# Kernel tuning notes

Hardware: AMD Instinct MI355X
Metric: run time of the kernel (lower is better)

The kernel has to match this reference:

```python
import jax, jax.numpy as jnp
import numpy as np
import math

B, S, D, H = 2, 2048, 1024, 16
HD = D // H  # 64 head features


def setup_inputs() -> dict:
    key = jax.random.key(0)
    ks = jax.random.split(key, 6)
    x = jax.random.normal(ks[0], (B, S, D), jnp.float32)
    wq = jax.random.normal(ks[1], (D, D), jnp.float32) * 0.02
    wk = jax.random.normal(ks[2], (D, D), jnp.float32) * 0.02
    wv = jax.random.normal(ks[3], (D, D), jnp.float32) * 0.02
    wo = jax.random.normal(ks[4], (D, D), jnp.float32) * 0.02
    # Llama-style RoPE frequencies: unit-modulus complex per (pos, pair),
    # stored as separate cos/sin arrays of shape [S, HD//2].
    inv_freq = 1.0 / (10000.0 ** (jnp.arange(0, HD, 2, dtype=jnp.float32) / HD))
    ang = jnp.arange(S, dtype=jnp.float32)[:, None] * inv_freq[None, :]
    freq_cos = jnp.cos(ang)
    freq_sin = jnp.sin(ang)
    # realistic padding: each sequence keeps a random prefix of at least S//2 tokens
    lengths = jax.random.randint(ks[5], (B,), S // 2, S + 1)
    padding_mask = (jnp.arange(S)[None, :] < lengths[:, None]).astype(jnp.int32)
    return dict(x=x, wq=wq, wk=wk, wv=wv, wo=wo,
                freq_cos=freq_cos, freq_sin=freq_sin, padding_mask=padding_mask)


def _apply_rope(t, cos, sin):
    # t: [B, S, H, HD]; cos/sin: [S, HD//2]
    tr = t.reshape(t.shape[:-1] + (HD // 2, 2))
    t0, t1 = tr[..., 0], tr[..., 1]
    c = cos[None, :, None, :]
    s = sin[None, :, None, :]
    o0 = t0 * c - t1 * s  # real part of complex multiply
    o1 = t0 * s + t1 * c  # imag part
    return jnp.stack([o0, o1], axis=-1).reshape(t.shape)


def reference(x, wq, wk, wv, wo, freq_cos, freq_sin, padding_mask):
    # QKV projections (torch Linear: y = x @ W.T, no bias)
    q = (x @ wq.T).reshape(B, S, H, HD)
    k = (x @ wk.T).reshape(B, S, H, HD)
    v = (x @ wv.T).reshape(B, S, H, HD)
    q = _apply_rope(q, freq_cos, freq_sin)
    k = _apply_rope(k, freq_cos, freq_sin)
    q = jnp.transpose(q, (0, 2, 1, 3))  # [B,H,S,HD]
    k = jnp.transpose(k, (0, 2, 1, 3))
    v = jnp.transpose(v, (0, 2, 1, 3))
    # NOTE: original scales by sqrt(n_features), not sqrt(head_dim)
    scores = jnp.einsum('bhqd,bhkd->bhqk', q, k) / math.sqrt(D)
    bias = jnp.where(padding_mask[:, None, None, :] == 0,
                     jnp.float32(-jnp.inf), jnp.float32(0.0))
    p = jax.nn.softmax(scores + bias, axis=-1)
    out = jnp.einsum('bhqk,bhkd->bhqd', p, v)
    out = jnp.transpose(out, (0, 2, 1, 3)).reshape(B, S, D)
    return out @ wo.T
```

## Files before the change

kernel.cpp:

```cpp
#include <hip/hip_runtime.h>
#include <hip/hip_bf16.h>
#include <stdint.h>

typedef unsigned short u16;
typedef __attribute__((ext_vector_type(8))) short bf16x8;
typedef __attribute__((ext_vector_type(4))) float f32x4;
typedef __attribute__((ext_vector_type(16))) float f32x16;

__device__ __forceinline__ u16 f2bf(float f) {
  union { float f; uint32_t u; } a; a.f = f;
  return (u16)((a.u + 0x7FFFu + ((a.u >> 16) & 1u)) >> 16);
}

__device__ __forceinline__ void gload_lds16(const void* g, void* l) {
  auto* gp = (__attribute__((address_space(1))) void*)(uintptr_t)g;
  auto* lp = (__attribute__((address_space(3))) void*)(uintptr_t)l;
  __builtin_amdgcn_global_load_lds(gp, lp, 16, 0, 0);
}

__device__ __forceinline__ float exp2_fast(float x) {
  float r;
  asm("v_exp_f32 %0, %1" : "=v"(r) : "v"(x));
  return r;
}

template <int N> __device__ __forceinline__ void waitvm() {
  if constexpr (N == 3)      asm volatile("s_waitcnt vmcnt(3)" ::: "memory");
  else if constexpr (N == 4) asm volatile("s_waitcnt vmcnt(4)" ::: "memory");
  else                       asm volatile("s_waitcnt vmcnt(0)" ::: "memory");
}

#define CVTPK(d, a, b) asm("v_cvt_pk_bf16_f32 %0, %1, %2" : "=v"(d) : "v"(a), "v"(b))
#define SWAP32(a, b)   asm("v_permlane32_swap_b32 %0, %1" : "+v"(a), "+v"(b))
#define BARRIER() do { asm volatile("" ::: "memory"); __builtin_amdgcn_s_barrier(); asm volatile("" ::: "memory"); } while (0)

__global__ void cvt_kernel(const float4* __restrict__ x, const float4* __restrict__ wq,
                           const float4* __restrict__ wk, const float4* __restrict__ wv,
                           const float4* __restrict__ wo,
                           ushort4* __restrict__ xb, ushort4* __restrict__ wqkv,
                           ushort4* __restrict__ wob) {
  const int XN = (2 * 2048 * 1024) / 4;
  const int WN = (1024 * 1024) / 4;
  const int total = XN + 4 * WN;
  for (int i = blockIdx.x * 256 + threadIdx.x; i < total; i += gridDim.x * 256) {
    float4 v; ushort4* dst;
    if (i < XN) { v = x[i]; dst = xb + i; }
    else {
      int j = i - XN; int m = j >> 18; int o = j & (WN - 1);
      const float4* src = (m == 0) ? wq : (m == 1) ? wk : (m == 2) ? wv : wo;
      v = src[o];
      dst = (m < 3) ? (wqkv + j) : (wob + o);
    }
    ushort4 r; r.x = f2bf(v.x); r.y = f2bf(v.y); r.z = f2bf(v.z); r.w = f2bf(v.w);
    *dst = r;
  }
}

__global__ void len_kernel(const int* __restrict__ mask, int* __restrict__ lens) {
  __shared__ int red[256];
  int b = blockIdx.x, s = 0;
  for (int i = threadIdx.x; i < 2048; i += 256) s += mask[b * 2048 + i];
  red[threadIdx.x] = s;
  __syncthreads();
  if (threadIdx.x < 64) {
    int v = red[threadIdx.x] + red[threadIdx.x + 64] + red[threadIdx.x + 128] + red[threadIdx.x + 192];
    #pragma unroll
    for (int o = 32; o > 0; o >>= 1) v += __shfl_down(v, o);
    if (threadIdx.x == 0) lens[b] = v;
  }
}

template <int BM, int BN, int MODE>
__global__ __launch_bounds__(256, 3)
void gemm3(const u16* __restrict__ A, const u16* __restrict__ Bm,
           int nTm, float* __restrict__ outf,
           u16* __restrict__ Qb, u16* __restrict__ Kb, u16* __restrict__ VbT,
           const float* __restrict__ cosT, const float* __restrict__ sinT) {
  constexpr int MREP = BM / 32;
  constexpr int NREP = BN / 32;
  constexpr int LA = BM / 64;
  constexpr int LB = BN / 64;
  constexpr int LOADS = LA + LB;
  __shared__ alignas(16) u16 SA[3][BM * 32];
  __shared__ alignas(16) u16 SB[3][BN * 32];

  const int tid = threadIdx.x, lane = tid & 63, wid = tid >> 6;
  const int wm = (wid >> 1) * (BM / 2), wn = (wid & 1) * (BN / 2);
  const int lr = lane & 15, lg = lane >> 4;

  const int cpx = gridDim.x >> 3;
  const int bid = (blockIdx.x & 7) * cpx + (blockIdx.x >> 3);
  const int m0 = (bid % nTm) * BM;
  const int n0 = (bid / nTm) * BN;

  const int srow = tid >> 2;
  const int schunk = (tid & 3) ^ ((srow >> 1) & 3);
  const u16* gA = A + (int64_t)(m0 + srow) * 1024 + schunk * 8;
  const u16* gB = Bm + (int64_t)(n0 + srow) * 1024 + schunk * 8;
  const int sdst = wid * 512;

#define STAGE(b, t) do { const int _ko = (t) * 32; \
    _Pragma("unroll") for (int j = 0; j < LA; ++j) \
      gload_lds16(gA + (int64_t)(j * 64) * 1024 + _ko, &SA[b][j * 2048 + sdst]); \
    _Pragma("unroll") for (int j = 0; j < LB; ++j) \
      gload_lds16(gB + (int64_t)(j * 64) * 1024 + _ko, &SB[b][j * 2048 + sdst]); } while (0)

  f32x4 acc[MREP][NREP];
  #pragma unroll
  for (int i = 0; i < MREP; ++i)
    #pragma unroll
    for (int j = 0; j < NREP; ++j)
      #pragma unroll
      for (int e = 0; e < 4; ++e) acc[i][j][e] = 0.0f;

  const int rchunk = (lg ^ ((lr >> 1) & 3)) * 8;

  STAGE(0, 0);
  STAGE(1, 1);
  waitvm<LOADS>();
  BARRIER();

  int bc = 0, bs = 2;
  for (int t = 0; t < 32; ++t) {
    if (t < 30) STAGE(bs, t + 2);
    const u16* sa = SA[bc];
    const u16* sb = SB[bc];
    bf16x8 af[MREP], bfm[NREP];
    #pragma unroll
    for (int i = 0; i < MREP; ++i) af[i] = *(const bf16x8*)&sa[(wm + i * 16 + lr) * 32 + rchunk];
    #pragma unroll
    for (int i = 0; i < NREP; ++i) bfm[i] = *(const bf16x8*)&sb[(wn + i * 16 + lr) * 32 + rchunk];
    #pragma unroll
    for (int mi = 0; mi < MREP; ++mi)
      #pragma unroll
      for (int ni = 0; ni < NREP; ++ni)
        acc[mi][ni] = __builtin_amdgcn_mfma_f32_16x16x32_bf16(af[mi], bfm[ni], acc[mi][ni], 0, 0, 0);
    if (t < 30) waitvm<LOADS>();
    else        waitvm<0>();
    BARRIER();
    bc = (bc == 2) ? 0 : bc + 1;
    bs = (bs == 2) ? 0 : bs + 1;
  }

  if (MODE == 0) {
    #pragma unroll
    for (int mi = 0; mi < MREP; ++mi)
      #pragma unroll
      for (int r = 0; r < 4; ++r) {
        const int row = m0 + wm + mi * 16 + lg * 4 + r;
        float* orow = outf + (int64_t)row * 1024 + n0 + wn + lr;
        #pragma unroll
        for (int ni = 0; ni < NREP; ++ni) orow[ni * 16] = acc[mi][ni][r];
      }
  } else {
    #pragma unroll
    for (int mi = 0; mi < MREP; ++mi) {
      #pragma unroll
      for (int r = 0; r < 4; ++r) {
        const int row = m0 + wm + mi * 16 + lg * 4 + r;
        const int bb = row >> 11, ss = row & 2047;
        #pragma unroll
        for (int ni = 0; ni < NREP; ++ni) {
          const int n = n0 + wn + ni * 16 + lr;
          float v = acc[mi][ni][r];
          if (n < 2048) {
            float partner = __shfl_xor(v, 1);
            const int ii = (n >> 1) & 31;
            const float c = cosT[ss * 32 + ii];
            const float sn = sinT[ss * 32 + ii];
            float rv = (n & 1) ? (partner * sn + v * c) : (v * c - partner * sn);
            const int h = (n >> 6) & 15, d = n & 63;
            const int idx = ((bb * 16 + h) * 2048 + ss) * 64 + d;
            if (n < 1024) Qb[idx] = f2bf(rv * 0.0450842298f);
            else          Kb[idx] = f2bf(rv);
          } else {
            const int n2 = n - 2048;
            const int h = n2 >> 6, d = n2 & 63;
            VbT[((int64_t)(bb * 16 + h) * 64 + d) * 2048 + ss] = f2bf(v);
          }
        }
      }
    }
  }
#undef STAGE
}

__global__ __launch_bounds__(256, 2)
void attn_kernel(const u16* __restrict__ Qb, const u16* __restrict__ Kb,
                 const u16* __restrict__ VbT, u16* __restrict__ attnb,
                 const int* __restrict__ lens) {
  __shared__ alignas(16) u16 Klds[2][64 * 64];
  __shared__ alignas(16) u16 Vlds[2][64 * 64];
  const int tid = threadIdx.x, lane = tid & 63, wid = tid >> 6;
  const int hi = lane >> 5, ql = lane & 31;
  const int bh = blockIdx.x >> 4;
  const int len = lens[bh >> 4];
  const int qrow = (blockIdx.x & 15) * 128 + wid * 32 + ql;

  bf16x8 qf[4];
  const u16* qptr = Qb + ((int64_t)bh * 2048 + qrow) * 64 + hi * 8;
  #pragma unroll
  for (int c = 0; c < 4; ++c) qf[c] = *(const bf16x8*)(qptr + c * 16);

  const int srow = tid >> 3, schunk = (tid & 7) ^ (srow & 7);
  const u16* kg = Kb + ((int64_t)bh * 2048 + srow) * 64 + schunk * 8;
  const u16* vg = VbT + ((int64_t)bh * 64 + srow) * 2048 + schunk * 8;
  const int dstoff = wid * 512;

  f32x16 oacc[2];
  #pragma unroll
  for (int r = 0; r < 16; ++r) { oacc[0][r] = 0.0f; oacc[1][r] = 0.0f; }
  float mrun = -1e30f, lrun = 0.0f;

  const int nt = (len + 63) >> 6;
  gload_lds16(kg,             &Klds[0][dstoff]);
  gload_lds16(kg + 32 * 64,   &Klds[0][2048 + dstoff]);
  gload_lds16(vg,             &Vlds[0][dstoff]);
  gload_lds16(vg + 32 * 2048, &Vlds[0][2048 + dstoff]);
  __syncthreads();

  const u16* kgn = kg + 64 * 64;
  const u16* vgn = vg + 64;

  for (int t = 0; t < nt; ++t) {
    const int bu = t & 1;
    if (t + 1 < nt) {
      gload_lds16(kgn,             &Klds[bu ^ 1][dstoff]);
      gload_lds16(kgn + 32 * 64,   &Klds[bu ^ 1][2048 + dstoff]);
      gload_lds16(vgn,             &Vlds[bu ^ 1][dstoff]);
      gload_lds16(vgn + 32 * 2048, &Vlds[bu ^ 1][2048 + dstoff]);
    }
    kgn += 64 * 64; vgn += 64;

    f32x16 s0, s1;
    #pragma unroll
    for (int r = 0; r < 16; ++r) { s0[r] = 0.0f; s1[r] = 0.0f; }
    __builtin_amdgcn_s_setprio(1);
    #pragma unroll
    for (int c = 0; c < 4; ++c) {
      const int slot = (((2 * c + hi) ^ (ql & 7)) * 8);
      bf16x8 kf0 = *(const bf16x8*)&Klds[bu][ql * 64 + slot];
      bf16x8 kf1 = *(const bf16x8*)&Klds[bu][(32 + ql) * 64 + slot];
      s0 = __builtin_amdgcn_mfma_f32_32x32x16_bf16(kf0, qf[c], s0, 0, 0, 0);
      s1 = __builtin_amdgcn_mfma_f32_32x32x16_bf16(kf1, qf[c], s1, 0, 0, 0);
    }
    __builtin_amdgcn_s_setprio(0);

    const int k0 = t * 64;
    if (k0 + 64 > len) {
      #pragma unroll
      for (int r = 0; r < 16; ++r) {
        const int key = k0 + (r & 3) + 8 * (r >> 2) + 4 * hi;
        if (key >= len) s0[r] = -1e30f;
        if (key + 32 >= len) s1[r] = -1e30f;
      }
    }

    float ma = fmaxf(s0[0], s1[0]), mb = fmaxf(s0[1], s1[1]);
    float mc = fmaxf(s0[2], s1[2]), md = fmaxf(s0[3], s1[3]);
    #pragma unroll
    for (int r = 4; r < 16; r += 4) {
      ma = fmaxf(ma, fmaxf(s0[r], s1[r]));
      mb = fmaxf(mb, fmaxf(s0[r + 1], s1[r + 1]));
      mc = fmaxf(mc, fmaxf(s0[r + 2], s1[r + 2]));
      md = fmaxf(md, fmaxf(s0[r + 3], s1[r + 3]));
    }
    float mx = fmaxf(fmaxf(ma, mb), fmaxf(mc, md));
    mx = fmaxf(mx, __shfl_xor(mx, 32));
    if (!__all(mx - mrun <= 11.0f)) {
      const float mnew = fmaxf(mrun, mx);
      const float sc = exp2_fast(mrun - mnew);
      #pragma unroll
      for (int r = 0; r < 16; ++r) { oacc[0][r] *= sc; oacc[1][r] *= sc; }
      lrun *= sc;
      mrun = mnew;
    }
    float p[32];
    float ps0 = 0.0f, ps1 = 0.0f, ps2 = 0.0f, ps3 = 0.0f;
    #pragma unroll
    for (int r = 0; r < 16; r += 4) {
      p[r]      = exp2_fast(s0[r] - mrun);
      p[r + 1]  = exp2_fast(s0[r + 1] - mrun);
      p[r + 2]  = exp2_fast(s0[r + 2] - mrun);
      p[r + 3]  = exp2_fast(s0[r + 3] - mrun);
      p[16 + r]     = exp2_fast(s1[r] - mrun);
      p[16 + r + 1] = exp2_fast(s1[r + 1] - mrun);
      p[16 + r + 2] = exp2_fast(s1[r + 2] - mrun);
      p[16 + r + 3] = exp2_fast(s1[r + 3] - mrun);
      ps0 += p[r] + p[16 + r];
      ps1 += p[r + 1] + p[16 + r + 1];
      ps2 += p[r + 2] + p[16 + r + 2];
      ps3 += p[r + 3] + p[16 + r + 3];
    }
    float psum = (ps0 + ps1) + (ps2 + ps3);
    psum += __shfl_xor(psum, 32);
    lrun += psum;

    bf16x8 pfrag[4];
    #pragma unroll
    for (int ks = 0; ks < 4; ++ks) {
      uint32_t a0, a1, a2, a3;
      CVTPK(a0, p[8 * ks + 0], p[8 * ks + 1]);
      CVTPK(a1, p[8 * ks + 2], p[8 * ks + 3]);
      CVTPK(a2, p[8 * ks + 4], p[8 * ks + 5]);
      CVTPK(a3, p[8 * ks + 6], p[8 * ks + 7]);
      SWAP32(a0, a2);
      SWAP32(a1, a3);
      union { uint32_t u[4]; bf16x8 v; } pw;
      pw.u[0] = a0; pw.u[1] = a1; pw.u[2] = a2; pw.u[3] = a3;
      pfrag[ks] = pw.v;
    }

    __builtin_amdgcn_s_setprio(1);
    #pragma unroll
    for (int dc = 0; dc < 2; ++dc) {
      const int drow = dc * 32 + ql;
      #pragma unroll
      for (int ks = 0; ks < 4; ++ks) {
        const int slot = (((2 * ks + hi) ^ (ql & 7)) * 8);
        bf16x8 vf = *(const bf16x8*)&Vlds[bu][drow * 64 + slot];
        oacc[dc] = __builtin_amdgcn_mfma_f32_32x32x16_bf16(vf, pfrag[ks], oacc[dc], 0, 0, 0);
      }
    }
    __builtin_amdgcn_s_setprio(0);
    __syncthreads();
  }

  const float inv = 1.0f / lrun;
  u16* outp = attnb + ((int64_t)((bh >> 4) * 2048 + qrow)) * 1024 + (bh & 15) * 64;
  #pragma unroll
  for (int dc = 0; dc < 2; ++dc)
    #pragma unroll
    for (int g = 0; g < 4; ++g) {
      ushort4 w;
      w.x = f2bf(oacc[dc][4 * g + 0] * inv);
      w.y = f2bf(oacc[dc][4 * g + 1] * inv);
      w.z = f2bf(oacc[dc][4 * g + 2] * inv);
      w.w = f2bf(oacc[dc][4 * g + 3] * inv);
      *(ushort4*)(outp + dc * 32 + 8 * g + 4 * hi) = w;
    }
}

extern "C" void kernel_launch(void* const* d_in, const int* in_sizes, int n_in,
                              void* d_out, int out_size, void* d_ws, size_t ws_size,
                              hipStream_t stream) {
  const float* x    = (const float*)d_in[0];
  const float* wq   = (const float*)d_in[1];
  const float* wk   = (const float*)d_in[2];
  const float* wv   = (const float*)d_in[3];
  const float* wo   = (const float*)d_in[4];
  const float* fcos = (const float*)d_in[5];
  const float* fsin = (const float*)d_in[6];
  const int*   pmsk = (const int*)d_in[7];
  float* out = (float*)d_out;

  char* ws = (char*)d_ws;
  u16* XB    = (u16*)(ws);
  u16* WQKV  = (u16*)(ws + (size_t)8  * 1048576);
  u16* WOB   = (u16*)(ws + (size_t)14 * 1048576);
  u16* QB    = (u16*)(ws + (size_t)16 * 1048576);
  u16* KB    = (u16*)(ws + (size_t)24 * 1048576);
  u16* VBT   = (u16*)(ws + (size_t)32 * 1048576);
  u16* ATTNB = (u16*)(ws + (size_t)40 * 1048576);
  int* LENS  = (int*)(ws + (size_t)48 * 1048576);

  cvt_kernel<<<2048, 256, 0, stream>>>((const float4*)x, (const float4*)wq,
                                       (const float4*)wk, (const float4*)wv,
                                       (const float4*)wo, (ushort4*)XB,
                                       (ushort4*)WQKV, (ushort4*)WOB);
  len_kernel<<<2, 256, 0, stream>>>(pmsk, LENS);

  gemm3<128, 128, 1><<<768, 256, 0, stream>>>(XB, WQKV, 32, nullptr,
                                              QB, KB, VBT, fcos, fsin);

  attn_kernel<<<512, 256, 0, stream>>>(QB, KB, VBT, ATTNB, LENS);

  gemm3<128, 64, 0><<<512, 256, 0, stream>>>(ATTNB, WOB, 32, out,
                                             nullptr, nullptr, nullptr, nullptr, nullptr);
}
```

Before: 121.5 us.

## Switch GEMMs to 32x32x16 MFMA and split V transpose into separate kernel

Both GEMM instantiations now use 32x32x16 bf16 MFMA tiles with 16-element accumulators instead of 16x16x32, so fewer LDS fragment loads are needed per MFMA. The QKV epilogue writes V in row-major head layout, which avoids the strided transposed scatter. A new vtrans kernel then transposes V into the layout attention expects using byte-permute register shuffles. This adds a kernel launch and an extra pass over V through global memory, and it reuses the attention output buffer as scratch.

Result: slower. 126.1 us (+3.8%).

```diff
diff --git a/kernel.cpp b/kernel.cpp
--- a/kernel.cpp
+++ b/kernel.cpp
@@ -72,12 +72,12 @@
 
 template <int BM, int BN, int MODE>
 __global__ __launch_bounds__(256, 3)
-void gemm3(const u16* __restrict__ A, const u16* __restrict__ Bm,
-           int nTm, float* __restrict__ outf,
-           u16* __restrict__ Qb, u16* __restrict__ Kb, u16* __restrict__ VbT,
-           const float* __restrict__ cosT, const float* __restrict__ sinT) {
-  constexpr int MREP = BM / 32;
-  constexpr int NREP = BN / 32;
+void gemm32(const u16* __restrict__ A, const u16* __restrict__ Bm,
+            int nTm, float* __restrict__ outf,
+            u16* __restrict__ Qb, u16* __restrict__ Kb, u16* __restrict__ Vb,
+            const float* __restrict__ cosT, const float* __restrict__ sinT) {
+  constexpr int MF = BM / 64;
+  constexpr int NF = BN / 64;
   constexpr int LA = BM / 64;
   constexpr int LB = BN / 64;
   constexpr int LOADS = LA + LB;
@@ -86,7 +86,7 @@
 
   const int tid = threadIdx.x, lane = tid & 63, wid = tid >> 6;
   const int wm = (wid >> 1) * (BM / 2), wn = (wid & 1) * (BN / 2);
-  const int lr = lane & 15, lg = lane >> 4;
+  const int l31 = lane & 31, hi = lane >> 5;
 
   const int cpx = gridDim.x >> 3;
   const int bid = (blockIdx.x & 7) * cpx + (blockIdx.x >> 3);
@@ -105,15 +105,13 @@
     _Pragma("unroll") for (int j = 0; j < LB; ++j) \
       gload_lds16(gB + (int64_t)(j * 64) * 1024 + _ko, &SB[b][j * 2048 + sdst]); } while (0)
 
-  f32x4 acc[MREP][NREP];
-  #pragma unroll
-  for (int i = 0; i < MREP; ++i)
-    #pragma unroll
-    for (int j = 0; j < NREP; ++j)
-      #pragma unroll
-      for (int e = 0; e < 4; ++e) acc[i][j][e] = 0.0f;
-
-  const int rchunk = (lg ^ ((lr >> 1) & 3)) * 8;
+  f32x16 acc[MF][NF];
+  #pragma unroll
+  for (int i = 0; i < MF; ++i)
+    #pragma unroll
+    for (int j = 0; j < NF; ++j)
+      #pragma unroll
+      for (int e = 0; e < 16; ++e) acc[i][j][e] = 0.0f;
 
   STAGE(0, 0);
   STAGE(1, 1);
@@ -125,16 +123,28 @@
     if (t < 30) STAGE(bs, t + 2);
     const u16* sa = SA[bc];
     const u16* sb = SB[bc];
-    bf16x8 af[MREP], bfm[NREP];
-    #pragma unroll
-    for (int i = 0; i < MREP; ++i) af[i] = *(const bf16x8*)&sa[(wm + i * 16 + lr) * 32 + rchunk];
-    #pragma unroll
-    for (int i = 0; i < NREP; ++i) bfm[i] = *(const bf16x8*)&sb[(wn + i * 16 + lr) * 32 + rchunk];
-    #pragma unroll
-    for (int mi = 0; mi < MREP; ++mi)
-      #pragma unroll
-      for (int ni = 0; ni < NREP; ++ni)
-        acc[mi][ni] = __builtin_amdgcn_mfma_f32_16x16x32_bf16(af[mi], bfm[ni], acc[mi][ni], 0, 0, 0);
+    bf16x8 af[MF][2], bfm[NF][2];
+    #pragma unroll
+    for (int mf = 0; mf < MF; ++mf)
+      #pragma unroll
+      for (int kh = 0; kh < 2; ++kh) {
+        const int row = wm + mf * 32 + l31;
+        af[mf][kh] = *(const bf16x8*)&sa[row * 32 + (((kh * 2 + hi) ^ ((row >> 1) & 3)) * 8)];
+      }
+    #pragma unroll
+    for (int nf = 0; nf < NF; ++nf)
+      #pragma unroll
+      for (int kh = 0; kh < 2; ++kh) {
+        const int row = wn + nf * 32 + l31;
+        bfm[nf][kh] = *(const bf16x8*)&sb[row * 32 + (((kh * 2 + hi) ^ ((row >> 1) & 3)) * 8)];
+      }
+    #pragma unroll
+    for (int kh = 0; kh < 2; ++kh)
+      #pragma unroll
+      for (int mf = 0; mf < MF; ++mf)
+        #pragma unroll
+        for (int nf = 0; nf < NF; ++nf)
+          acc[mf][nf] = __builtin_amdgcn_mfma_f32_32x32x16_bf16(af[mf][kh], bfm[nf][kh], acc[mf][nf], 0, 0, 0);
     if (t < 30) waitvm<LOADS>();
     else        waitvm<0>();
     BARRIER();
@@ -144,45 +154,66 @@
 
   if (MODE == 0) {
     #pragma unroll
-    for (int mi = 0; mi < MREP; ++mi)
-      #pragma unroll
-      for (int r = 0; r < 4; ++r) {
-        const int row = m0 + wm + mi * 16 + lg * 4 + r;
-        float* orow = outf + (int64_t)row * 1024 + n0 + wn + lr;
+    for (int mf = 0; mf < MF; ++mf)
+      #pragma unroll
+      for (int reg = 0; reg < 16; ++reg) {
+        const int row = m0 + wm + mf * 32 + (reg & 3) + 8 * (reg >> 2) + 4 * hi;
+        float* orow = outf + (int64_t)row * 1024 + n0 + wn + l31;
         #pragma unroll
-        for (int ni = 0; ni < NREP; ++ni) orow[ni * 16] = acc[mi][ni][r];
+        for (int nf = 0; nf < NF; ++nf) orow[nf * 32] = acc[mf][nf][reg];
       }
   } else {
     #pragma unroll
-    for (int mi = 0; mi < MREP; ++mi) {
-      #pragma unroll
-      for (int r = 0; r < 4; ++r) {
-        const int row = m0 + wm + mi * 16 + lg * 4 + r;
+    for (int mf = 0; mf < MF; ++mf) {
+      #pragma unroll
+      for (int reg = 0; reg < 16; ++reg) {
+        const int row = m0 + wm + mf * 32 + (reg & 3) + 8 * (reg >> 2) + 4 * hi;
         const int bb = row >> 11, ss = row & 2047;
         #pragma unroll
-        for (int ni = 0; ni < NREP; ++ni) {
-          const int n = n0 + wn + ni * 16 + lr;
-          float v = acc[mi][ni][r];
+        for (int nf = 0; nf < NF; ++nf) {
+          const int n = n0 + wn + nf * 32 + l31;
+          float v = acc[mf][nf][reg];
+          const int h = (n >> 6) & 15, d = n & 63;
+          const int idx = ((bb * 16 + h) * 2048 + ss) * 64 + d;
           if (n < 2048) {
             float partner = __shfl_xor(v, 1);
             const int ii = (n >> 1) & 31;
             const float c = cosT[ss * 32 + ii];
             const float sn = sinT[ss * 32 + ii];
             float rv = (n & 1) ? (partner * sn + v * c) : (v * c - partner * sn);
-            const int h = (n >> 6) & 15, d = n & 63;
-            const int idx = ((bb * 16 + h) * 2048 + ss) * 64 + d;
             if (n < 1024) Qb[idx] = f2bf(rv * 0.0450842298f);
             else          Kb[idx] = f2bf(rv);
           } else {
-            const int n2 = n - 2048;
-            const int h = n2 >> 6, d = n2 & 63;
-            VbT[((int64_t)(bb * 16 + h) * 64 + d) * 2048 + ss] = f2bf(v);
+            Vb[idx] = f2bf(v);
           }
         }
       }
     }
   }
 #undef STAGE
+}
+
+__global__ __launch_bounds__(256)
+void vtrans(const u16* __restrict__ VB, u16* __restrict__ VbT) {
+  const int bh = blockIdx.x >> 3, s0 = (blockIdx.x & 7) * 256;
+  const int t = threadIdx.x;
+  const int d8 = (t & 7) * 8;
+  const int s8 = s0 + (t >> 3) * 8;
+  const u16* src = VB + ((int64_t)bh * 2048 + s8) * 64 + d8;
+  uint32_t r[8][4];
+  #pragma unroll
+  for (int j = 0; j < 8; ++j) *(uint4*)&r[j][0] = *(const uint4*)(src + j * 64);
+  uint32_t w[8][4];
+  #pragma unroll
+  for (int rp = 0; rp < 4; ++rp)
+    #pragma unroll
+    for (int k = 0; k < 4; ++k) {
+      w[2 * k][rp]     = __builtin_amdgcn_perm(r[2 * rp + 1][k], r[2 * rp][k], 0x05040100u);
+      w[2 * k + 1][rp] = __builtin_amdgcn_perm(r[2 * rp + 1][k], r[2 * rp][k], 0x07060302u);
+    }
+  u16* dst = VbT + ((int64_t)bh * 64 + d8) * 2048 + s8;
+  #pragma unroll
+  for (int i = 0; i < 8; ++i) *(uint4*)(dst + (int64_t)i * 2048) = *(uint4*)&w[i][0];
 }
 
 __global__ __launch_bounds__(256, 2)
@@ -363,6 +394,7 @@
   u16* VBT   = (u16*)(ws + (size_t)32 * 1048576);
   u16* ATTNB = (u16*)(ws + (size_t)40 * 1048576);
   int* LENS  = (int*)(ws + (size_t)48 * 1048576);
+  u16* VB    = ATTNB;
 
   cvt_kernel<<<2048, 256, 0, stream>>>((const float4*)x, (const float4*)wq,
                                        (const float4*)wk, (const float4*)wv,
@@ -370,11 +402,13 @@
                                        (ushort4*)WQKV, (ushort4*)WOB);
   len_kernel<<<2, 256, 0, stream>>>(pmsk, LENS);
 
-  gemm3<128, 128, 1><<<768, 256, 0, stream>>>(XB, WQKV, 32, nullptr,
-                                              QB, KB, VBT, fcos, fsin);
+  gemm32<128, 128, 1><<<768, 256, 0, stream>>>(XB, WQKV, 32, nullptr,
+                                               QB, KB, VB, fcos, fsin);
+
+  vtrans<<<256, 256, 0, stream>>>(VB, VBT);
 
   attn_kernel<<<512, 256, 0, stream>>>(QB, KB, VBT, ATTNB, LENS);
 
-  gemm3<128, 64, 0><<<512, 256, 0, stream>>>(ATTNB, WOB, 32, out,
-                                             nullptr, nullptr, nullptr, nullptr, nullptr);
-}
+  gemm32<128, 64, 0><<<512, 256, 0, stream>>>(ATTNB, WOB, 32, out,
+                                              nullptr, nullptr, nullptr, nullptr, nullptr);
+}
```
